# Performance work log

Measured on AMD Instinct MI355X. Metric: run time of the kernel, lower is better.

## Reference

```python
import jax, jax.numpy as jnp
import numpy as np

B, H, FEAT = 16384, 256, 256
GX, GY, SW = 70, 70, 2


def setup_inputs() -> dict:
    key = jax.random.key(0)
    ks = jax.random.split(key, 10)
    stdv = 1.0 / np.sqrt(H)
    feats = jax.random.normal(ks[0], (B, FEAT), dtype=jnp.float32)
    coords = jax.random.randint(ks[1], (B, 2), 0, 64).astype(jnp.float32)
    input_tensor = jnp.concatenate([feats, coords], axis=1)  # [B, FEAT+2]
    hidden = jax.random.normal(ks[2], (B, H), dtype=jnp.float32)
    u = lambda k, shp: jax.random.uniform(k, shp, jnp.float32, -stdv, stdv)
    return {
        "input_tensor": input_tensor,
        "hidden": hidden,
        "w_ih": u(ks[3], (4 * H, FEAT)),
        "b_ih": u(ks[4], (4 * H,)),
        "w_hh": u(ks[5], (4 * H, H)),
        "b_hh": u(ks[6], (4 * H,)),
        "w_out": u(ks[7], (H, 2 * H)),
        "b_out": u(ks[8], (H,)),
        "memory": jax.random.normal(ks[9], (GX, GY, H), dtype=jnp.float32) * 0.1,
    }


def reference(input_tensor, hidden, w_ih, b_ih, w_hh, b_hh, w_out, b_out, memory):
    feature = input_tensor[:, :-2]
    grid = input_tensor[:, -2:].astype(jnp.int32) + SW  # [B,2]

    gi = feature @ w_ih.T + b_ih  # [B,4H]
    gh = hidden @ w_hh.T + b_hh   # [B,4H]
    i_r, i_i, i_n, i_s = jnp.split(gi, 4, axis=1)
    h_r, h_i, h_n, h_s = jnp.split(gh, 4, axis=1)

    resetgate = jax.nn.sigmoid(i_r + h_r)
    updategate = jax.nn.sigmoid(i_i + h_i)
    spatialgate = jax.nn.sigmoid(i_s + h_s)
    newgate = jnp.tanh(i_n + resetgate * h_n)

    # gather (2*SW+1)^2 neighborhood per sample from spatial memory
    gx = jnp.clip(grid[:, 0], 0, GX - 1)
    gy = jnp.clip(grid[:, 1], 0, GY - 1)
    off = jnp.arange(-SW, SW + 1)  # [K]
    xi = jnp.clip(gx[:, None] + off[None, :], 0, GX - 1)  # [B,K]
    yi = jnp.clip(gy[:, None] + off[None, :], 0, GY - 1)  # [B,K]
    K = 2 * SW + 1
    x_flat = jnp.broadcast_to(xi[:, :, None], (xi.shape[0], K, K)).reshape(xi.shape[0], -1)
    y_flat = jnp.broadcast_to(yi[:, None, :], (yi.shape[0], K, K)).reshape(yi.shape[0], -1)
    context = memory[x_flat, y_flat]  # [B, K*K, H]

    # attention (query is detached in original)
    q = jax.lax.stop_gradient(newgate)  # [B,H]
    attn = jnp.einsum('bh,bkh->bk', q, context)  # [B, K*K]
    attn = jnp.where(attn == 0, -jnp.inf, attn)
    w = jax.nn.softmax(attn, axis=1)
    w = jnp.where(jnp.isnan(w), 0.0, w)
    mix = jnp.einsum('bk,bkh->bh', w, context)  # [B,H]
    combined = jnp.concatenate([mix, q], axis=1)  # [B,2H]
    atten_cs = jnp.tanh(combined @ w_out.T + b_out)  # [B,H]

    curr_state = newgate + spatialgate * atten_cs
    output = curr_state + updategate * (hidden - curr_state)
    return output
```

## Files before the change

### kernel.cpp

```cpp
#include <hip/hip_runtime.h>
#include <stdint.h>

#define B_N 16384
#define H_N 256
#define IN_W 258
#define GX_N 70
#define GY_N 70
#define SW_N 2
#define KK_N 25

typedef __bf16 bf16x8 __attribute__((ext_vector_type(8)));
typedef __bf16 bf16x4 __attribute__((ext_vector_type(4)));
typedef __bf16 bf16x2 __attribute__((ext_vector_type(2)));
typedef float f32x4 __attribute__((ext_vector_type(4)));

#define AS1 __attribute__((address_space(1)))
#define AS3 __attribute__((address_space(3)))

static __device__ __forceinline__ void gload16(const void* g, void* l) {
    __builtin_amdgcn_global_load_lds((const AS1 uint32_t*)g, (AS3 uint32_t*)l, 16, 0, 0);
}

#define E_AB   8388608ULL
#define E_WF   8912896ULL
#define E_WOUT 9043968ULL
#define E_COMB 9043968ULL
#define E_UGSG 17432576ULL

__global__ __launch_bounds__(256) void cast_kernel(
    const float* __restrict__ in_t, const float* __restrict__ hid,
    const float* __restrict__ wih, const float* __restrict__ whh,
    const float* __restrict__ wout, __bf16* __restrict__ dst)
{
    size_t g = (size_t)blockIdx.x * blockDim.x + threadIdx.x;
    size_t stride = (size_t)gridDim.x * blockDim.x;
    for (size_t e = g * 4; e < E_WOUT; e += stride * 4) {
        const float* src;
        if (e < E_AB) {
            size_t row = e >> 9;
            size_t c = e & 511;
            src = (c < 256) ? (in_t + row * IN_W + c) : (hid + row * 256 + (c - 256));
        } else if (e < E_WF) {
            size_t off = e - E_AB;
            size_t j = off >> 9;
            size_t k = off & 511;
            size_t c = j >> 8;
            size_t col = j & 255;
            size_t base = (c == 0) ? 0 : (c == 1) ? 256 : (c == 2) ? 768 : 512;
            const float* srcm = (k < 256) ? wih : whh;
            src = srcm + (base + col) * 256 + (k & 255);
        } else {
            src = wout + (e - E_WF);
        }
        bf16x4 o;
        o.x = (__bf16)src[0];
        o.y = (__bf16)src[1];
        o.z = (__bf16)src[2];
        o.w = (__bf16)src[3];
        *reinterpret_cast<bf16x4*>(dst + e) = o;
    }
}

__global__ __launch_bounds__(256, 2) void gates_gemm(
    const __bf16* __restrict__ AB, const __bf16* __restrict__ wfull,
    const float* __restrict__ b_ih, const float* __restrict__ b_hh,
    __bf16* __restrict__ comb, __bf16* __restrict__ ugsg)
{
    __shared__ __bf16 ldsA[2][8192];
    __shared__ __bf16 ldsB[2][4096];
    const int t = threadIdx.x;
    const int lane = t & 63, w = t >> 6;
    const int lr = lane & 15, seg = lane >> 4;
    const int rb = blockIdx.x * 256;
    const int h0 = blockIdx.y * 32;

    const __bf16* gAt = AB + (size_t)(rb + t) * 512;
    const int bc = (t & 127) >> 5;
    const int bcol = t & 31;
    const __bf16* gBt = wfull + (size_t)(bc * 256 + h0 + bcol) * 512 + ((t >> 7) << 3);
    __bf16* lA0 = &ldsA[0][t * 8];
    __bf16* lA1 = &ldsA[1][t * 8];
    __bf16* lB0 = &ldsB[0][t * 8];
    __bf16* lB1 = &ldsB[1][t * 8];

    f32x4 acc[4][6], accni[4][2], accnh[4][2];
#pragma unroll
    for (int rh = 0; rh < 4; rh++) {
#pragma unroll
        for (int cn = 0; cn < 6; cn++) acc[rh][cn] = (f32x4){0.f, 0.f, 0.f, 0.f};
        accni[rh][0] = (f32x4){0.f, 0.f, 0.f, 0.f};
        accni[rh][1] = (f32x4){0.f, 0.f, 0.f, 0.f};
        accnh[rh][0] = (f32x4){0.f, 0.f, 0.f, 0.f};
        accnh[rh][1] = (f32x4){0.f, 0.f, 0.f, 0.f};
    }

    gload16(gAt + 0, lA0);
    gload16(gAt + 8, lA0 + 2048);
    gload16(gAt + 16, lA0 + 4096);
    gload16(gAt + 24, lA0 + 6144);
    gload16(gBt + 0, lB0);
    gload16(gBt + 16, lB0 + 2048);
    __syncthreads();

#pragma unroll 1
    for (int tt = 0; tt < 16; tt++) {
        const int cur = tt & 1;
        if (tt < 15) {
            const int kn = (tt + 1) * 32;
            __bf16* la = cur ? lA0 : lA1;
            __bf16* lb = cur ? lB0 : lB1;
            gload16(gAt + kn, la);
            gload16(gAt + kn + 8, la + 2048);
            gload16(gAt + kn + 16, la + 4096);
            gload16(gAt + kn + 24, la + 6144);
            gload16(gBt + kn, lb);
            gload16(gBt + kn + 16, lb + 2048);
        }
        const __bf16* cA = ldsA[cur];
        const __bf16* cB = ldsB[cur];
        bf16x8 af[4];
#pragma unroll
        for (int rh = 0; rh < 4; rh++)
            af[rh] = *reinterpret_cast<const bf16x8*>(cA + seg * 2048 + (w * 64 + rh * 16 + lr) * 8);
#pragma unroll
        for (int cn = 0; cn < 6; cn++) {
            bf16x8 bb = *reinterpret_cast<const bf16x8*>(cB + seg * 1024 + (cn * 16 + lr) * 8);
#pragma unroll
            for (int rh = 0; rh < 4; rh++)
                acc[rh][cn] = __builtin_amdgcn_mfma_f32_16x16x32_bf16(af[rh], bb, acc[rh][cn], 0, 0, 0);
        }
        bf16x8 b6 = *reinterpret_cast<const bf16x8*>(cB + seg * 1024 + (96 + lr) * 8);
        bf16x8 b7 = *reinterpret_cast<const bf16x8*>(cB + seg * 1024 + (112 + lr) * 8);
        if (tt < 8) {
#pragma unroll
            for (int rh = 0; rh < 4; rh++) {
                accni[rh][0] = __builtin_amdgcn_mfma_f32_16x16x32_bf16(af[rh], b6, accni[rh][0], 0, 0, 0);
                accni[rh][1] = __builtin_amdgcn_mfma_f32_16x16x32_bf16(af[rh], b7, accni[rh][1], 0, 0, 0);
            }
        } else {
#pragma unroll
            for (int rh = 0; rh < 4; rh++) {
                accnh[rh][0] = __builtin_amdgcn_mfma_f32_16x16x32_bf16(af[rh], b6, accnh[rh][0], 0, 0, 0);
                accnh[rh][1] = __builtin_amdgcn_mfma_f32_16x16x32_bf16(af[rh], b7, accnh[rh][1], 0, 0, 0);
            }
        }
        __syncthreads();
    }

#pragma unroll
    for (int hh = 0; hh < 2; hh++) {
        const int col = h0 + hh * 16 + lr;
        const float br_ = b_ih[col] + b_hh[col];
        const float bi_ = b_ih[col + 256] + b_hh[col + 256];
        const float bs_ = b_ih[col + 768] + b_hh[col + 768];
        const float bni = b_ih[col + 512];
        const float bnh = b_hh[col + 512];
#pragma unroll
        for (int rh = 0; rh < 4; rh++) {
#pragma unroll
            for (int r = 0; r < 4; r++) {
                const int row = rb + w * 64 + rh * 16 + seg * 4 + r;
                float sr = acc[rh][hh][r] + br_;
                float si = acc[rh][2 + hh][r] + bi_;
                float ss = acc[rh][4 + hh][r] + bs_;
                float vni = accni[rh][hh][r] + bni;
                float vnh = accnh[rh][hh][r] + bnh;
                float rg = 1.f / (1.f + __expf(-sr));
                float ug = 1.f / (1.f + __expf(-si));
                float sg = 1.f / (1.f + __expf(-ss));
                float ng = tanhf(vni + rg * vnh);
                comb[(size_t)row * 512 + 256 + col] = (__bf16)ng;
                bf16x2 us;
                us.x = (__bf16)ug;
                us.y = (__bf16)sg;
                *reinterpret_cast<bf16x2*>(ugsg + ((size_t)row * 256 + col) * 2) = us;
            }
        }
    }
}

__global__ __launch_bounds__(256) void attn_kernel(
    const float* __restrict__ in_t, const float* __restrict__ memory,
    __bf16* __restrict__ comb)
{
    const int w = threadIdx.x >> 6;
    const int lane = threadIdx.x & 63;
    const int b = blockIdx.x * 4 + w;
    const float* row_in = in_t + (size_t)b * IN_W;
    int gx = (int)row_in[256] + SW_N;
    int gy = (int)row_in[257] + SW_N;
    gx = min(max(gx, 0), GX_N - 1);
    gy = min(max(gy, 0), GY_N - 1);

    bf16x4 qb = *reinterpret_cast<const bf16x4*>(comb + (size_t)b * 512 + 256 + lane * 4);
    float q0 = (float)qb.x, q1 = (float)qb.y, q2 = (float)qb.z, q3 = (float)qb.w;

    float m = -INFINITY, d = 0.f;
    float o0 = 0.f, o1 = 0.f, o2 = 0.f, o3 = 0.f;
#pragma unroll
    for (int k = 0; k < KK_N; k++) {
        int i = k / 5, j = k % 5;
        int xi = min(max(gx + i - SW_N, 0), GX_N - 1);
        int yj = min(max(gy + j - SW_N, 0), GY_N - 1);
        const f32x4* cp = reinterpret_cast<const f32x4*>(memory + ((size_t)xi * GY_N + yj) * H_N);
        f32x4 v = cp[lane];
        float p = q0 * v.x + q1 * v.y + q2 * v.z + q3 * v.w;
        for (int off = 32; off; off >>= 1) p += __shfl_xor(p, off, 64);
        float a = (p == 0.f) ? -INFINITY : p;
        float mn = fmaxf(m, a);
        if (mn != -INFINITY) {
            float alpha = __expf(m - mn);
            float e = __expf(a - mn);
            d = d * alpha + e;
            o0 = o0 * alpha + e * v.x;
            o1 = o1 * alpha + e * v.y;
            o2 = o2 * alpha + e * v.z;
            o3 = o3 * alpha + e * v.w;
            m = mn;
        }
    }
    float inv = (d != 0.f) ? 1.f / d : 0.f;
    bf16x4 ob;
    ob.x = (__bf16)(o0 * inv);
    ob.y = (__bf16)(o1 * inv);
    ob.z = (__bf16)(o2 * inv);
    ob.w = (__bf16)(o3 * inv);
    *reinterpret_cast<bf16x4*>(comb + (size_t)b * 512 + lane * 4) = ob;
}

__global__ __launch_bounds__(256, 4) void out_gemm(
    const __bf16* __restrict__ comb, const __bf16* __restrict__ woB,
    const float* __restrict__ b_out, const __bf16* __restrict__ ugsg,
    const float* __restrict__ hidden, float* __restrict__ out)
{
    __shared__ __bf16 ldsA[2][4096];
    __shared__ __bf16 ldsB[2][2048];
    const int t = threadIdx.x;
    const int lane = t & 63, w = t >> 6;
    const int lr = lane & 15, seg = lane >> 4;
    const int rb = blockIdx.x * 128;
    const int n0 = blockIdx.y * 64;

    const __bf16* gAt = comb + (size_t)(rb + (t & 127)) * 512 + ((t >> 7) << 3);
    const __bf16* gBt = woB + (size_t)(n0 + (t & 63)) * 512 + ((t >> 6) << 3);
    __bf16* lA0 = &ldsA[0][t * 8];
    __bf16* lA1 = &ldsA[1][t * 8];
    __bf16* lB0 = &ldsB[0][t * 8];
    __bf16* lB1 = &ldsB[1][t * 8];

    f32x4 acc[2][4];
#pragma unroll
    for (int rh = 0; rh < 2; rh++)
#pragma unroll
        for (int ct = 0; ct < 4; ct++) acc[rh][ct] = (f32x4){0.f, 0.f, 0.f, 0.f};

    gload16(gAt + 0, lA0);
    gload16(gAt + 16, lA0 + 2048);
    gload16(gBt + 0, lB0);
    __syncthreads();

#pragma unroll 1
    for (int tt = 0; tt < 16; tt++) {
        const int cur = tt & 1;
        if (tt < 15) {
            const int kn = (tt + 1) * 32;
            __bf16* la = cur ? lA0 : lA1;
            __bf16* lb = cur ? lB0 : lB1;
            gload16(gAt + kn, la);
            gload16(gAt + kn + 16, la + 2048);
            gload16(gBt + kn, lb);
        }
        const __bf16* cA = ldsA[cur];
        const __bf16* cB = ldsB[cur];
        bf16x8 af[2];
#pragma unroll
        for (int rh = 0; rh < 2; rh++)
            af[rh] = *reinterpret_cast<const bf16x8*>(cA + seg * 1024 + (w * 32 + rh * 16 + lr) * 8);
#pragma unroll
        for (int ct = 0; ct < 4; ct++) {
            bf16x8 bb = *reinterpret_cast<const bf16x8*>(cB + seg * 512 + (ct * 16 + lr) * 8);
#pragma unroll
            for (int rh = 0; rh < 2; rh++)
                acc[rh][ct] = __builtin_amdgcn_mfma_f32_16x16x32_bf16(af[rh], bb, acc[rh][ct], 0, 0, 0);
        }
        __syncthreads();
    }

#pragma unroll
    for (int ct = 0; ct < 4; ct++) {
        int col = n0 + ct * 16 + lr;
        float bo = b_out[col];
#pragma unroll
        for (int rh = 0; rh < 2; rh++) {
#pragma unroll
            for (int r = 0; r < 4; r++) {
                int row = rb + w * 32 + rh * 16 + seg * 4 + r;
                size_t idx = (size_t)row * 256 + col;
                float acs = tanhf(acc[rh][ct][r] + bo);
                float ng = (float)comb[(size_t)row * 512 + 256 + col];
                bf16x2 us = *reinterpret_cast<const bf16x2*>(ugsg + idx * 2);
                float ug = (float)us.x, sg = (float)us.y;
                float curr = ng + sg * acs;
                out[idx] = curr + ug * (hidden[idx] - curr);
            }
        }
    }
}

extern "C" void kernel_launch(void* const* d_in, const int* in_sizes, int n_in,
                              void* d_out, int out_size, void* d_ws, size_t ws_size,
                              hipStream_t stream) {
    const float* input_t = (const float*)d_in[0];
    const float* hidden  = (const float*)d_in[1];
    const float* w_ih    = (const float*)d_in[2];
    const float* b_ih    = (const float*)d_in[3];
    const float* w_hh    = (const float*)d_in[4];
    const float* b_hh    = (const float*)d_in[5];
    const float* w_out   = (const float*)d_in[6];
    const float* b_out   = (const float*)d_in[7];
    const float* memory  = (const float*)d_in[8];
    float* out = (float*)d_out;

    __bf16* base  = (__bf16*)d_ws;
    __bf16* AB    = base;
    __bf16* wfull = base + E_AB;
    __bf16* woutB = base + E_WF;
    __bf16* comb  = base + E_COMB;
    __bf16* ugsg  = base + E_UGSG;

    cast_kernel<<<4096, 256, 0, stream>>>(input_t, hidden, w_ih, w_hh, w_out, base);
    gates_gemm<<<dim3(64, 8), 256, 0, stream>>>(AB, wfull, b_ih, b_hh, comb, ugsg);
    attn_kernel<<<4096, 256, 0, stream>>>(input_t, memory, comb);
    out_gemm<<<dim3(128, 4), 256, 0, stream>>>(comb, woutB, b_out, ugsg, hidden, out);
}
```

Before: 205.8 us.

## Triple-buffer LDS staging in both GEMMs with vmcnt-based waits and setprio

Both GEMM kernels move from double to triple-buffered LDS tiles and prefetch two K-tiles ahead. Each loop step now uses one barrier after a partial vmcnt wait instead of a full syncthreads at the end, which is meant to keep more global-to-LDS loads in flight while the MFMA work runs. s_setprio raises wave priority around the MFMA block. This costs more LDS per block (gates_gemm grows to about 72KB), which may cut occupancy below the launch_bounds target of 2 blocks per CU. The hand-written vmcnt counts also depend on the compiler not issuing other vector memory ops inside the loop.

Measured after the change: 205.6 us. Within noise of the previous version (-0.1%).

```diff
diff --git a/kernel.cpp b/kernel.cpp
--- a/kernel.cpp
+++ b/kernel.cpp
@@ -66,8 +66,8 @@
     const float* __restrict__ b_ih, const float* __restrict__ b_hh,
     __bf16* __restrict__ comb, __bf16* __restrict__ ugsg)
 {
-    __shared__ __bf16 ldsA[2][8192];
-    __shared__ __bf16 ldsB[2][4096];
+    __shared__ __bf16 ldsA[3][8192];
+    __shared__ __bf16 ldsB[3][4096];
     const int t = threadIdx.x;
     const int lane = t & 63, w = t >> 6;
     const int lr = lane & 15, seg = lane >> 4;
@@ -78,10 +78,6 @@
     const int bc = (t & 127) >> 5;
     const int bcol = t & 31;
     const __bf16* gBt = wfull + (size_t)(bc * 256 + h0 + bcol) * 512 + ((t >> 7) << 3);
-    __bf16* lA0 = &ldsA[0][t * 8];
-    __bf16* lA1 = &ldsA[1][t * 8];
-    __bf16* lB0 = &ldsB[0][t * 8];
-    __bf16* lB1 = &ldsB[1][t * 8];
 
     f32x4 acc[4][6], accni[4][2], accnh[4][2];
 #pragma unroll
@@ -94,34 +90,38 @@
         accnh[rh][1] = (f32x4){0.f, 0.f, 0.f, 0.f};
     }
 
-    gload16(gAt + 0, lA0);
-    gload16(gAt + 8, lA0 + 2048);
-    gload16(gAt + 16, lA0 + 4096);
-    gload16(gAt + 24, lA0 + 6144);
-    gload16(gBt + 0, lB0);
-    gload16(gBt + 16, lB0 + 2048);
-    __syncthreads();
-
+#define G_STAGE(TILE, BUF)                                         \
+    do {                                                           \
+        const int kn_ = (TILE) * 32;                               \
+        __bf16* la_ = &ldsA[(BUF)][t * 8];                         \
+        __bf16* lb_ = &ldsB[(BUF)][t * 8];                         \
+        gload16(gAt + kn_, la_);                                   \
+        gload16(gAt + kn_ + 8, la_ + 2048);                        \
+        gload16(gAt + kn_ + 16, la_ + 4096);                       \
+        gload16(gAt + kn_ + 24, la_ + 6144);                       \
+        gload16(gBt + kn_, lb_);                                   \
+        gload16(gBt + kn_ + 16, lb_ + 2048);                       \
+    } while (0)
+
+    G_STAGE(0, 0);
+    G_STAGE(1, 1);
+
+    int cur = 0, nxt2 = 2;
 #pragma unroll 1
     for (int tt = 0; tt < 16; tt++) {
-        const int cur = tt & 1;
-        if (tt < 15) {
-            const int kn = (tt + 1) * 32;
-            __bf16* la = cur ? lA0 : lA1;
-            __bf16* lb = cur ? lB0 : lB1;
-            gload16(gAt + kn, la);
-            gload16(gAt + kn + 8, la + 2048);
-            gload16(gAt + kn + 16, la + 4096);
-            gload16(gAt + kn + 24, la + 6144);
-            gload16(gBt + kn, lb);
-            gload16(gBt + kn + 16, lb + 2048);
-        }
+        if (tt < 15) asm volatile("s_waitcnt vmcnt(6)" ::: "memory");
+        else         asm volatile("s_waitcnt vmcnt(0)" ::: "memory");
+        __builtin_amdgcn_s_barrier();
+        if (tt < 14) G_STAGE(tt + 2, nxt2);
+
         const __bf16* cA = ldsA[cur];
         const __bf16* cB = ldsB[cur];
         bf16x8 af[4];
 #pragma unroll
         for (int rh = 0; rh < 4; rh++)
             af[rh] = *reinterpret_cast<const bf16x8*>(cA + seg * 2048 + (w * 64 + rh * 16 + lr) * 8);
+
+        __builtin_amdgcn_s_setprio(1);
 #pragma unroll
         for (int cn = 0; cn < 6; cn++) {
             bf16x8 bb = *reinterpret_cast<const bf16x8*>(cB + seg * 1024 + (cn * 16 + lr) * 8);
@@ -144,8 +144,12 @@
                 accnh[rh][1] = __builtin_amdgcn_mfma_f32_16x16x32_bf16(af[rh], b7, accnh[rh][1], 0, 0, 0);
             }
         }
-        __syncthreads();
-    }
+        __builtin_amdgcn_s_setprio(0);
+
+        cur = (cur == 2) ? 0 : cur + 1;
+        nxt2 = (nxt2 == 2) ? 0 : nxt2 + 1;
+    }
+#undef G_STAGE
 
 #pragma unroll
     for (int hh = 0; hh < 2; hh++) {
@@ -233,8 +237,8 @@
     const float* __restrict__ b_out, const __bf16* __restrict__ ugsg,
     const float* __restrict__ hidden, float* __restrict__ out)
 {
-    __shared__ __bf16 ldsA[2][4096];
-    __shared__ __bf16 ldsB[2][2048];
+    __shared__ __bf16 ldsA[3][4096];
+    __shared__ __bf16 ldsB[3][2048];
     const int t = threadIdx.x;
     const int lane = t & 63, w = t >> 6;
     const int lr = lane & 15, seg = lane >> 4;
@@ -243,10 +247,6 @@
 
     const __bf16* gAt = comb + (size_t)(rb + (t & 127)) * 512 + ((t >> 7) << 3);
     const __bf16* gBt = woB + (size_t)(n0 + (t & 63)) * 512 + ((t >> 6) << 3);
-    __bf16* lA0 = &ldsA[0][t * 8];
-    __bf16* lA1 = &ldsA[1][t * 8];
-    __bf16* lB0 = &ldsB[0][t * 8];
-    __bf16* lB1 = &ldsB[1][t * 8];
 
     f32x4 acc[2][4];
 #pragma unroll
@@ -254,28 +254,34 @@
 #pragma unroll
         for (int ct = 0; ct < 4; ct++) acc[rh][ct] = (f32x4){0.f, 0.f, 0.f, 0.f};
 
-    gload16(gAt + 0, lA0);
-    gload16(gAt + 16, lA0 + 2048);
-    gload16(gBt + 0, lB0);
-    __syncthreads();
-
+#define O_STAGE(TILE, BUF)                                         \
+    do {                                                           \
+        const int kn_ = (TILE) * 32;                               \
+        __bf16* la_ = &ldsA[(BUF)][t * 8];                         \
+        __bf16* lb_ = &ldsB[(BUF)][t * 8];                         \
+        gload16(gAt + kn_, la_);                                   \
+        gload16(gAt + kn_ + 16, la_ + 2048);                       \
+        gload16(gBt + kn_, lb_);                                   \
+    } while (0)
+
+    O_STAGE(0, 0);
+    O_STAGE(1, 1);
+
+    int cur = 0, nxt2 = 2;
 #pragma unroll 1
     for (int tt = 0; tt < 16; tt++) {
-        const int cur = tt & 1;
-        if (tt < 15) {
-            const int kn = (tt + 1) * 32;
-            __bf16* la = cur ? lA0 : lA1;
-            __bf16* lb = cur ? lB0 : lB1;
-            gload16(gAt + kn, la);
-            gload16(gAt + kn + 16, la + 2048);
-            gload16(gBt + kn, lb);
-        }
+        if (tt < 15) asm volatile("s_waitcnt vmcnt(3)" ::: "memory");
+        else         asm volatile("s_waitcnt vmcnt(0)" ::: "memory");
+        __builtin_amdgcn_s_barrier();
+        if (tt < 14) O_STAGE(tt + 2, nxt2);
+
         const __bf16* cA = ldsA[cur];
         const __bf16* cB = ldsB[cur];
         bf16x8 af[2];
 #pragma unroll
         for (int rh = 0; rh < 2; rh++)
             af[rh] = *reinterpret_cast<const bf16x8*>(cA + seg * 1024 + (w * 32 + rh * 16 + lr) * 8);
+        __builtin_amdgcn_s_setprio(1);
 #pragma unroll
         for (int ct = 0; ct < 4; ct++) {
             bf16x8 bb = *reinterpret_cast<const bf16x8*>(cB + seg * 512 + (ct * 16 + lr) * 8);
@@ -283,8 +289,12 @@
             for (int rh = 0; rh < 2; rh++)
                 acc[rh][ct] = __builtin_amdgcn_mfma_f32_16x16x32_bf16(af[rh], bb, acc[rh][ct], 0, 0, 0);
         }
-        __syncthreads();
-    }
+        __builtin_amdgcn_s_setprio(0);
+
+        cur = (cur == 2) ? 0 : cur + 1;
+        nxt2 = (nxt2 == 2) ? 0 : nxt2 + 1;
+    }
+#undef O_STAGE
 
 #pragma unroll
     for (int ct = 0; ct < 4; ct++) {
```
